# Kernel optimization log

Measured on AMD Instinct MI355X. Metric: run time of the kernel, lower is better.

Reference implementation:

```python
import jax, jax.numpy as jnp
import numpy as np
from jax import lax

THRESH = 0.8
LENS = 0.4
DECAY = 0.2
LOG_SIG_MIN, LOG_SIG_MAX = -20.0, 2.0
WINS = 15

@jax.custom_vjp
def act_fun(x):
    return (x > THRESH).astype(x.dtype)

def _act_fwd(x):
    return act_fun(x), x

def _act_bwd(x, g):
    return (g * (jnp.abs(x - THRESH) < LENS).astype(g.dtype),)

act_fun.defvjp(_act_fwd, _act_bwd)

B, NIN, HID, NACT = 2048, 512, 1024, 32

def _xavier(key, out_d, in_d):
    lim = jnp.sqrt(6.0 / (in_d + out_d)).astype(jnp.float32)
    return jax.random.uniform(key, (out_d, in_d), jnp.float32, -lim, lim)

def setup_inputs() -> dict:
    key = jax.random.key(0)
    ks = jax.random.split(key, 12)
    inp = {
        'state': jax.random.normal(ks[0], (B, 5, NIN), jnp.float32),
        'w1': _xavier(ks[1], HID, NIN), 'b1': jnp.zeros((HID,), jnp.float32),
        'w2': _xavier(ks[2], HID, NIN), 'b2': jnp.zeros((HID,), jnp.float32),
        'w3': _xavier(ks[3], HID, NIN), 'b3': jnp.zeros((HID,), jnp.float32),
        'wl': _xavier(ks[4], 1, 3), 'bl': jnp.zeros((1,), jnp.float32),
        'w11': _xavier(ks[5], HID, 4 * HID), 'b11': jnp.zeros((HID,), jnp.float32),
        'w12': _xavier(ks[6], HID, HID), 'b12': jnp.zeros((HID,), jnp.float32),
        'w21': _xavier(ks[7], HID, 4 * HID), 'b21': jnp.zeros((HID,), jnp.float32),
        'w22': _xavier(ks[8], HID, HID), 'b22': jnp.zeros((HID,), jnp.float32),
        'wm': _xavier(ks[9], NACT, HID), 'bm': jnp.zeros((NACT,), jnp.float32),
        'ws': _xavier(ks[10], NACT, HID), 'bs': jnp.zeros((NACT,), jnp.float32),
    }
    return inp

def _policy_forward(state, w1, b1, w2, b2, w3, b3, wl, bl,
                    w11, b11, w12, b12, w21, b21, w22, b22, wm, bm, ws, bs):
    batch = state.shape[0]
    hid = w1.shape[0]
    seq = jnp.repeat(state, 3, axis=1)
    mem0 = jnp.zeros((batch, hid, 4), state.dtype)
    sp0 = jnp.zeros((batch, hid, 4), state.dtype)

    def step(carry, x_t):
        mem, spike = carry
        i1 = x_t @ w1.T + b1  # [B, HID]
        i2 = x_t @ w2.T + b2
        i3 = x_t @ w3.T + b3
        inner = jnp.einsum('bck,k->bc', mem[:, :, :3], wl[0]) + bl[0]
        inp_all = jnp.stack([i1, i2, i3, inner], axis=-1)  # [B, HID, 4]
        mem1 = mem * DECAY * (1.0 - spike) + inp_all
        sp1 = act_fun(mem1)
        return (mem1, sp1), sp1

    _, spikes = lax.scan(step, (mem0, sp0), jnp.swapaxes(seq, 0, 1))  # [T,B,HID,4]
    spikes = jnp.transpose(spikes, (1, 0, 2, 3)).reshape(batch, WINS, hid * 4)
    x = jnp.mean(spikes, axis=1)  # [B, 4*HID]

    x1 = jax.nn.relu(x @ w11.T + b11)
    x1 = jax.nn.relu(x1 @ w12.T + b12)
    mean = x1 @ wm.T + bm

    x2 = jax.nn.relu(x @ w21.T + b21)
    x2 = jax.nn.relu(x2 @ w22.T + b22)
    log_std = jnp.clip(x2 @ ws.T + bs, LOG_SIG_MIN, LOG_SIG_MAX)
    return mean, log_std

def reference(state, w1, b1, w2, b2, w3, b3, wl, bl,
              w11, b11, w12, b12, w21, b21, w22, b22, wm, bm, ws, bs):
    return _policy_forward(state, w1, b1, w2, b2, w3, b3, wl, bl,
                           w11, b11, w12, b12, w21, b21, w22, b22, wm, bm, ws, bs)
```

## Files before the change

kernel.cpp:

```cpp
#include <hip/hip_runtime.h>
#include <cstddef>
#include <cstdint>

#define THRESH 0.8f
#define DECAY  0.2f

typedef unsigned short ushort_t;
typedef __attribute__((ext_vector_type(8))) short bf16x8;
typedef __attribute__((ext_vector_type(4))) float f32x4;

__device__ __forceinline__ ushort_t f2bf(float f) {
    union { float f; unsigned u; } v; v.f = f;
    unsigned r = v.u + 0x7FFFu + ((v.u >> 16) & 1u);
    return (ushort_t)(r >> 16);
}
__device__ __forceinline__ float bf2f(ushort_t h) {
    union { unsigned u; float f; } v; v.u = ((unsigned)h) << 16;
    return v.f;
}
__device__ __forceinline__ float blo(unsigned u) {
    union { unsigned x; float f; } v; v.x = u << 16; return v.f;
}
__device__ __forceinline__ float bhi(unsigned u) {
    union { unsigned x; float f; } v; v.x = u & 0xFFFF0000u; return v.f;
}

__device__ __forceinline__ void gload16(const void* g, void* l) {
    __builtin_amdgcn_global_load_lds(
        (const __attribute__((address_space(1))) void*)g,
        (__attribute__((address_space(3))) void*)l,
        16, 0, 0);
}

__global__ __launch_bounds__(512) void cur_gemm512(
    const ushort_t* __restrict__ Ah, const ushort_t* __restrict__ Al,
    const ushort_t* __restrict__ Wh, const ushort_t* __restrict__ Wl,
    const float* __restrict__ bias, float* __restrict__ C,
    int K, int ldc)
{
    __shared__ ushort_t sA[2][128 * 32];
    __shared__ ushort_t sW[2][128 * 32];

    const int t = threadIdx.x;
    const int mBase = blockIdx.x * 128;
    const int nBase = blockIdx.y * 128;

    const int lane = t & 63;
    const int wv = t >> 6;
    const int wm = (wv & 1) * 64;
    const int wn = (wv >> 1) * 32;
    const int fr = lane & 15;
    const int fq = lane >> 4;
    const int fsw = (fq ^ ((fr >> 2) & 3)) * 8;

    const int r0 = t >> 2;
    const int cSw = ((t & 3) ^ ((r0 >> 2) & 3)) * 8;

    f32x4 acc[4][2];
#pragma unroll
    for (int i = 0; i < 4; i++)
#pragma unroll
        for (int j = 0; j < 2; j++) {
            f32x4 z = {0.f, 0.f, 0.f, 0.f};
            acc[i][j] = z;
        }

    for (int k0 = 0; k0 < K; k0 += 32) {
        const int lin = t * 8;
        gload16(&Ah[(size_t)(mBase + r0) * K + k0 + cSw], &sA[0][lin]);
        gload16(&Wh[(size_t)(nBase + r0) * K + k0 + cSw], &sW[0][lin]);
        gload16(&Al[(size_t)(mBase + r0) * K + k0 + cSw], &sA[1][lin]);
        gload16(&Wl[(size_t)(nBase + r0) * K + k0 + cSw], &sW[1][lin]);
        __syncthreads();

        bf16x8 af[4][2], wf[2][2];
#pragma unroll
        for (int s = 0; s < 2; s++) {
#pragma unroll
            for (int i = 0; i < 4; i++)
                af[i][s] = *(const bf16x8*)&sA[s][(wm + i * 16 + fr) * 32 + fsw];
#pragma unroll
            for (int j = 0; j < 2; j++)
                wf[j][s] = *(const bf16x8*)&sW[s][(wn + j * 16 + fr) * 32 + fsw];
        }
#pragma unroll
        for (int i = 0; i < 4; i++)
#pragma unroll
            for (int j = 0; j < 2; j++) {
                acc[i][j] = __builtin_amdgcn_mfma_f32_16x16x32_bf16(af[i][0], wf[j][0], acc[i][j], 0, 0, 0);
                acc[i][j] = __builtin_amdgcn_mfma_f32_16x16x32_bf16(af[i][0], wf[j][1], acc[i][j], 0, 0, 0);
                acc[i][j] = __builtin_amdgcn_mfma_f32_16x16x32_bf16(af[i][1], wf[j][0], acc[i][j], 0, 0, 0);
            }
        __syncthreads();
    }

#pragma unroll
    for (int j = 0; j < 2; j++) {
        const int col = nBase + wn + j * 16 + fr;
        const float bv = bias[col];
#pragma unroll
        for (int i = 0; i < 4; i++)
#pragma unroll
            for (int r = 0; r < 4; r++) {
                const int row = mBase + wm + i * 16 + fq * 4 + r;
                C[(size_t)row * ldc + col] = acc[i][j][r] + bv;
            }
    }
}

__global__ __launch_bounds__(256) void mlp_gemm256(
    const ushort_t* __restrict__ A, const ushort_t* __restrict__ W,
    float* __restrict__ C,
    int N, int K, int lda, int ldw, int ldc, int aHalfOff,
    size_t sliceStride)
{
    __shared__ ushort_t sA[128 * 32];
    __shared__ ushort_t sW[128 * 32];

    const int t = threadIdx.x;
    const int mBase = blockIdx.x * 128;
    const int nBase = blockIdx.y * 128;
    const int kOff = blockIdx.z * K;
    const int aOff = (2 * nBase >= N) ? aHalfOff : 0;
    float* Cz = C + (size_t)blockIdx.z * sliceStride;

    const int lane = t & 63;
    const int wv = t >> 6;
    const int wm = (wv & 1) * 64;
    const int wn = (wv >> 1) * 64;
    const int fr = lane & 15;
    const int fq = lane >> 4;
    const int fsw = (fq ^ ((fr >> 2) & 3)) * 8;

    const int r0 = t >> 2;
    const int cSw = ((t & 3) ^ ((r0 >> 2) & 3)) * 8;

    f32x4 acc[4][4];
#pragma unroll
    for (int i = 0; i < 4; i++)
#pragma unroll
        for (int j = 0; j < 4; j++) {
            f32x4 z = {0.f, 0.f, 0.f, 0.f};
            acc[i][j] = z;
        }

    for (int k0 = 0; k0 < K; k0 += 32) {
        gload16(&A[(size_t)(mBase + r0) * lda + aOff + kOff + k0 + cSw], &sA[t * 8]);
        gload16(&A[(size_t)(mBase + 64 + r0) * lda + aOff + kOff + k0 + cSw], &sA[2048 + t * 8]);
        gload16(&W[(size_t)(nBase + r0) * ldw + kOff + k0 + cSw], &sW[t * 8]);
        gload16(&W[(size_t)(nBase + 64 + r0) * ldw + kOff + k0 + cSw], &sW[2048 + t * 8]);
        __syncthreads();

        bf16x8 af[4], wf[4];
#pragma unroll
        for (int i = 0; i < 4; i++) {
            af[i] = *(const bf16x8*)&sA[(wm + i * 16 + fr) * 32 + fsw];
            wf[i] = *(const bf16x8*)&sW[(wn + i * 16 + fr) * 32 + fsw];
        }
#pragma unroll
        for (int i = 0; i < 4; i++)
#pragma unroll
            for (int j = 0; j < 4; j++)
                acc[i][j] = __builtin_amdgcn_mfma_f32_16x16x32_bf16(af[i], wf[j], acc[i][j], 0, 0, 0);
        __syncthreads();
    }

#pragma unroll
    for (int j = 0; j < 4; j++) {
        const int col = nBase + wn + j * 16 + fr;
#pragma unroll
        for (int i = 0; i < 4; i++)
#pragma unroll
            for (int r = 0; r < 4; r++) {
                const int row = mBase + wm + i * 16 + fq * 4 + r;
                Cz[(size_t)row * ldc + col] = acc[i][j][r];
            }
    }
}

template <int S>
__global__ __launch_bounds__(256) void reduce_relu(
    const float* __restrict__ part, const float* __restrict__ bias,
    ushort_t* __restrict__ out, int N, size_t MN)
{
    const size_t stride = (size_t)gridDim.x * 1024;
    for (size_t e = ((size_t)blockIdx.x * 256 + threadIdx.x) * 4; e < MN; e += stride) {
        float4 a = *(const float4*)&part[e];
#pragma unroll
        for (int s = 1; s < S; s++) {
            const float4 b = *(const float4*)&part[s * MN + e];
            a.x += b.x; a.y += b.y; a.z += b.z; a.w += b.w;
        }
        const int n = (int)(e & (size_t)(N - 1));
        const float4 bv = *(const float4*)&bias[n];
        ushort4 o;
        o.x = f2bf(fmaxf(a.x + bv.x, 0.f));
        o.y = f2bf(fmaxf(a.y + bv.y, 0.f));
        o.z = f2bf(fmaxf(a.z + bv.z, 0.f));
        o.w = f2bf(fmaxf(a.w + bv.w, 0.f));
        *(ushort4*)&out[e] = o;
    }
}

__global__ __launch_bounds__(256) void recur_kernel(
    const float* __restrict__ cur, const float* __restrict__ wl,
    const float* __restrict__ bl, ushort_t* __restrict__ x)
{
    const int idx = blockIdx.x * 256 + threadIdx.x;
    const int b = idx >> 10, c = idx & 1023;
    const float wl0 = wl[0], wl1 = wl[1], wl2 = wl[2], bl0 = bl[0];
    float m0 = 0, m1 = 0, m2 = 0, m3 = 0;
    float s0 = 0, s1 = 0, s2 = 0, s3 = 0;
#pragma unroll
    for (int f = 0; f < 5; f++) {
        const float* p = cur + (size_t)(b * 5 + f) * 3072 + c;
        const float i1 = p[0], i2 = p[1024], i3 = p[2048];
#pragma unroll
        for (int rep = 0; rep < 3; rep++) {
            const float inner = m0 * wl0 + m1 * wl1 + m2 * wl2 + bl0;
            const float n0 = i1 + ((m0 > THRESH) ? 0.f : DECAY * m0);
            const float n1 = i2 + ((m1 > THRESH) ? 0.f : DECAY * m1);
            const float n2 = i3 + ((m2 > THRESH) ? 0.f : DECAY * m2);
            const float n3 = inner + ((m3 > THRESH) ? 0.f : DECAY * m3);
            m0 = n0; m1 = n1; m2 = n2; m3 = n3;
            s0 += (n0 > THRESH) ? 1.f : 0.f;
            s1 += (n1 > THRESH) ? 1.f : 0.f;
            s2 += (n2 > THRESH) ? 1.f : 0.f;
            s3 += (n3 > THRESH) ? 1.f : 0.f;
        }
    }
    const float inv = 1.f / 15.f;
    ushort4 o;
    o.x = f2bf(s0 * inv); o.y = f2bf(s1 * inv);
    o.z = f2bf(s2 * inv); o.w = f2bf(s3 * inv);
    *(ushort4*)&x[(size_t)b * 4096 + c * 4] = o;
}

__device__ __forceinline__ void do_split4(const float4* src, ushort4* hi,
                                          ushort4* lo, int base, int t) {
#pragma unroll
    for (int p = 0; p < 4; p++) {
        const int i = base * 1024 + p * 256 + t;
        const float4 v = src[i];
        ushort4 h, l;
        h.x = f2bf(v.x); l.x = f2bf(v.x - bf2f(h.x));
        h.y = f2bf(v.y); l.y = f2bf(v.y - bf2f(h.y));
        h.z = f2bf(v.z); l.z = f2bf(v.z - bf2f(h.z));
        h.w = f2bf(v.w); l.w = f2bf(v.w - bf2f(h.w));
        hi[i] = h; lo[i] = l;
    }
}
__device__ __forceinline__ void do_cvt4(const float4* src, ushort4* dst,
                                        int base, int t) {
#pragma unroll
    for (int p = 0; p < 4; p++) {
        const int i = base * 1024 + p * 256 + t;
        const float4 v = src[i];
        ushort4 h;
        h.x = f2bf(v.x); h.y = f2bf(v.y); h.z = f2bf(v.z); h.w = f2bf(v.w);
        dst[i] = h;
    }
}

__global__ __launch_bounds__(256) void prep_kernel(
    const float* __restrict__ state,
    const float* __restrict__ w1, const float* __restrict__ w2,
    const float* __restrict__ w3,
    const float* __restrict__ w11, const float* __restrict__ w21,
    const float* __restrict__ w12, const float* __restrict__ w22,
    const float* __restrict__ b1, const float* __restrict__ b2,
    const float* __restrict__ b3, const float* __restrict__ b11,
    const float* __restrict__ b21, const float* __restrict__ b12,
    const float* __restrict__ b22,
    ushort_t* __restrict__ sh, ushort_t* __restrict__ sl,
    ushort_t* __restrict__ wh123, ushort_t* __restrict__ wl123,
    ushort_t* __restrict__ w1b, ushort_t* __restrict__ w2b,
    float* __restrict__ b123, float* __restrict__ bb1, float* __restrict__ bb2)
{
    const int bid = blockIdx.x;
    const int t = threadIdx.x;
    if (bid < 1280) {
        do_split4((const float4*)state, (ushort4*)sh, (ushort4*)sl, bid, t);
    } else if (bid < 1408) {
        do_split4((const float4*)w1, (ushort4*)wh123, (ushort4*)wl123, bid - 1280, t);
    } else if (bid < 1536) {
        do_split4((const float4*)w2, (ushort4*)(wh123 + 524288),
                  (ushort4*)(wl123 + 524288), bid - 1408, t);
    } else if (bid < 1664) {
        do_split4((const float4*)w3, (ushort4*)(wh123 + 1048576),
                  (ushort4*)(wl123 + 1048576), bid - 1536, t);
    } else if (bid < 2688) {
        do_cvt4((const float4*)w11, (ushort4*)w1b, bid - 1664, t);
    } else if (bid < 3712) {
        do_cvt4((const float4*)w21, (ushort4*)(w1b + 4194304), bid - 2688, t);
    } else if (bid < 3968) {
        do_cvt4((const float4*)w12, (ushort4*)w2b, bid - 3712, t);
    } else if (bid < 4224) {
        do_cvt4((const float4*)w22, (ushort4*)(w2b + 1048576), bid - 3968, t);
    } else {
#pragma unroll
        for (int p = 0; p < 4; p++) {
            const int i = p * 256 + t;
            b123[i] = b1[i]; b123[1024 + i] = b2[i]; b123[2048 + i] = b3[i];
            bb1[i] = b11[i]; bb1[1024 + i] = b21[i];
            bb2[i] = b12[i]; bb2[1024 + i] = b22[i];
        }
    }
}

__global__ __launch_bounds__(256) void head_kernel(
    const ushort_t* __restrict__ h, const float* __restrict__ wm,
    const float* __restrict__ bm, const float* __restrict__ ws,
    const float* __restrict__ bs, float* __restrict__ out)
{
    const int t = threadIdx.x;
    const int branch = blockIdx.x >> 8;
    const int n = t & 31;
    const int b = (blockIdx.x & 255) * 8 + (t >> 5);
    const ushort_t* hr = h + (size_t)b * 2048 + branch * 1024;
    const float* wr = (branch ? ws : wm) + (size_t)n * 1024;
    float s = 0.f;
#pragma unroll 4
    for (int k = 0; k < 1024; k += 8) {
        const uint4 hv = *(const uint4*)&hr[k];
        const float4 w0 = *(const float4*)&wr[k];
        const float4 w1 = *(const float4*)&wr[k + 4];
        s += blo(hv.x) * w0.x + bhi(hv.x) * w0.y
           + blo(hv.y) * w0.z + bhi(hv.y) * w0.w
           + blo(hv.z) * w1.x + bhi(hv.z) * w1.y
           + blo(hv.w) * w1.z + bhi(hv.w) * w1.w;
    }
    s += (branch ? bs : bm)[n];
    if (branch) s = fminf(fmaxf(s, -20.f), 2.f);
    out[(size_t)branch * 65536 + (size_t)b * 32 + n] = s;
}

extern "C" void kernel_launch(void* const* d_in, const int* in_sizes, int n_in,
                              void* d_out, int out_size, void* d_ws, size_t ws_size,
                              hipStream_t stream)
{
    const float* state = (const float*)d_in[0];
    const float* w1  = (const float*)d_in[1];  const float* b1  = (const float*)d_in[2];
    const float* w2  = (const float*)d_in[3];  const float* b2  = (const float*)d_in[4];
    const float* w3  = (const float*)d_in[5];  const float* b3  = (const float*)d_in[6];
    const float* wl  = (const float*)d_in[7];  const float* bl  = (const float*)d_in[8];
    const float* w11 = (const float*)d_in[9];  const float* b11 = (const float*)d_in[10];
    const float* w12 = (const float*)d_in[11]; const float* b12 = (const float*)d_in[12];
    const float* w21 = (const float*)d_in[13]; const float* b21 = (const float*)d_in[14];
    const float* w22 = (const float*)d_in[15]; const float* b22 = (const float*)d_in[16];
    const float* wm  = (const float*)d_in[17]; const float* bm  = (const float*)d_in[18];
    const float* ws  = (const float*)d_in[19]; const float* bs  = (const float*)d_in[20];
    float* out = (float*)d_out;

    char* wp = (char*)d_ws;
    float*    cur   = (float*)wp;     wp += (size_t)10240 * 3072 * 4;
    ushort_t* sh    = (ushort_t*)wp;  wp += (size_t)10240 * 512 * 2;
    ushort_t* sl    = (ushort_t*)wp;  wp += (size_t)10240 * 512 * 2;
    ushort_t* wh123 = (ushort_t*)wp;  wp += (size_t)3072 * 512 * 2;
    ushort_t* wl123 = (ushort_t*)wp;  wp += (size_t)3072 * 512 * 2;
    ushort_t* xb    = (ushort_t*)wp;  wp += (size_t)2048 * 4096 * 2;
    ushort_t* w1b   = (ushort_t*)wp;  wp += (size_t)2048 * 4096 * 2;
    ushort_t* w2b   = (ushort_t*)wp;  wp += (size_t)2048 * 1024 * 2;
    ushort_t* h1    = (ushort_t*)wp;  wp += (size_t)2048 * 2048 * 2;
    ushort_t* h2    = (ushort_t*)wp;  wp += (size_t)2048 * 2048 * 2;
    float*    b123  = (float*)wp;     wp += 3072 * 4;
    float*    bb1   = (float*)wp;     wp += 2048 * 4;
    float*    bb2   = (float*)wp;     wp += 2048 * 4;

    const size_t MN = (size_t)2048 * 2048;

    prep_kernel<<<4225, 256, 0, stream>>>(
        state, w1, w2, w3, w11, w21, w12, w22,
        b1, b2, b3, b11, b21, b12, b22,
        sh, sl, wh123, wl123, w1b, w2b, b123, bb1, bb2);

    cur_gemm512<<<dim3(80, 24), 512, 0, stream>>>(
        sh, sl, wh123, wl123, b123, cur, 512, 3072);

    recur_kernel<<<8192, 256, 0, stream>>>(cur, wl, bl, xb);

    mlp_gemm256<<<dim3(16, 16, 2), 256, 0, stream>>>(
        xb, w1b, cur, 2048, 2048, 4096, 4096, 2048, 0, MN);
    reduce_relu<2><<<1024, 256, 0, stream>>>(cur, bb1, h1, 2048, MN);

    mlp_gemm256<<<dim3(16, 16, 2), 256, 0, stream>>>(
        h1, w2b, cur, 2048, 512, 2048, 1024, 2048, 1024, MN);
    reduce_relu<2><<<1024, 256, 0, stream>>>(cur, bb2, h2, 2048, MN);

    head_kernel<<<512, 256, 0, stream>>>(h2, wm, bm, ws, bs, out);
}
```

Before: 435.6 us.

## Fuse input-current GEMM with spiking recurrence and drop LDS swizzle in MLP GEMM

The split-bf16 GEMM that produces the three input currents is merged with the LIF recurrence. Each block computes a 320-row by 96-column tile (64 batch rows × 5 frames, 32 channels × 3 weights) and runs the recurrence from shared memory, so the large fp32 `cur` tensor is never written to or read back from global memory. This removes a kernel launch and the intermediate traffic. In exchange the new tile shape gives lower MFMA reuse per block, the epilogue serialises four staging passes through LDS with barriers, and the LDS layout has no XOR swizzle, so bank conflicts are possible. Separately, the XOR swizzle in the MLP GEMM's LDS layout is replaced with a plain linear layout, which may add bank conflicts.

```diff
diff --git a/kernel.cpp b/kernel.cpp
--- a/kernel.cpp
+++ b/kernel.cpp
@@ -32,79 +32,128 @@
         16, 0, 0);
 }
 
-__global__ __launch_bounds__(512) void cur_gemm512(
+__global__ __launch_bounds__(512) void cur_recur_fused(
     const ushort_t* __restrict__ Ah, const ushort_t* __restrict__ Al,
     const ushort_t* __restrict__ Wh, const ushort_t* __restrict__ Wl,
-    const float* __restrict__ bias, float* __restrict__ C,
-    int K, int ldc)
-{
-    __shared__ ushort_t sA[2][128 * 32];
-    __shared__ ushort_t sW[2][128 * 32];
+    const float* __restrict__ b123, const float* __restrict__ wl,
+    const float* __restrict__ bl, ushort_t* __restrict__ x)
+{
+    __shared__ ushort_t smem[26624];
+    ushort_t* sAh = smem;
+    ushort_t* sAl = smem + 10240;
+    ushort_t* sWh = smem + 20480;
+    ushort_t* sWl = smem + 23552;
 
     const int t = threadIdx.x;
-    const int mBase = blockIdx.x * 128;
-    const int nBase = blockIdx.y * 128;
-
     const int lane = t & 63;
     const int wv = t >> 6;
-    const int wm = (wv & 1) * 64;
-    const int wn = (wv >> 1) * 32;
+    const int cBase = blockIdx.x * 32;
+    const int bBase = blockIdx.y * 64;
+    const int aRow0 = bBase * 5;
+
+    const int mg = wv & 3;
+    const int ng = wv >> 2;
     const int fr = lane & 15;
     const int fq = lane >> 4;
-    const int fsw = (fq ^ ((fr >> 2) & 3)) * 8;
-
-    const int r0 = t >> 2;
-    const int cSw = ((t & 3) ^ ((r0 >> 2) & 3)) * 8;
-
-    f32x4 acc[4][2];
-#pragma unroll
-    for (int i = 0; i < 4; i++)
-#pragma unroll
-        for (int j = 0; j < 2; j++) {
+    const int rlane = lane >> 2;
+    const int klane = (lane & 3) * 8;
+
+    f32x4 acc[5][3];
+#pragma unroll
+    for (int i = 0; i < 5; i++)
+#pragma unroll
+        for (int j = 0; j < 3; j++) {
             f32x4 z = {0.f, 0.f, 0.f, 0.f};
             acc[i][j] = z;
         }
 
-    for (int k0 = 0; k0 < K; k0 += 32) {
-        const int lin = t * 8;
-        gload16(&Ah[(size_t)(mBase + r0) * K + k0 + cSw], &sA[0][lin]);
-        gload16(&Wh[(size_t)(nBase + r0) * K + k0 + cSw], &sW[0][lin]);
-        gload16(&Al[(size_t)(mBase + r0) * K + k0 + cSw], &sA[1][lin]);
-        gload16(&Wl[(size_t)(nBase + r0) * K + k0 + cSw], &sW[1][lin]);
-        __syncthreads();
-
-        bf16x8 af[4][2], wf[2][2];
-#pragma unroll
-        for (int s = 0; s < 2; s++) {
-#pragma unroll
-            for (int i = 0; i < 4; i++)
-                af[i][s] = *(const bf16x8*)&sA[s][(wm + i * 16 + fr) * 32 + fsw];
-#pragma unroll
-            for (int j = 0; j < 2; j++)
-                wf[j][s] = *(const bf16x8*)&sW[s][(wn + j * 16 + fr) * 32 + fsw];
-        }
-#pragma unroll
-        for (int i = 0; i < 4; i++)
-#pragma unroll
-            for (int j = 0; j < 2; j++) {
-                acc[i][j] = __builtin_amdgcn_mfma_f32_16x16x32_bf16(af[i][0], wf[j][0], acc[i][j], 0, 0, 0);
-                acc[i][j] = __builtin_amdgcn_mfma_f32_16x16x32_bf16(af[i][0], wf[j][1], acc[i][j], 0, 0, 0);
-                acc[i][j] = __builtin_amdgcn_mfma_f32_16x16x32_bf16(af[i][1], wf[j][0], acc[i][j], 0, 0, 0);
+    for (int k0 = 0; k0 < 512; k0 += 32) {
+        for (int s = wv; s < 52; s += 8) {
+            if (s < 40) {
+                const int ss = (s < 20) ? s : s - 20;
+                const ushort_t* src = (s < 20) ? Ah : Al;
+                ushort_t* dst = (s < 20) ? sAh : sAl;
+                const int row = aRow0 + ss * 16 + rlane;
+                gload16(&src[(size_t)row * 512 + k0 + klane], &dst[ss * 512 + lane * 8]);
+            } else {
+                const int ss = (s < 46) ? s - 40 : s - 46;
+                const ushort_t* src = (s < 46) ? Wh : Wl;
+                ushort_t* dst = (s < 46) ? sWh : sWl;
+                const int wrow = ss * 16 + rlane;
+                const int row = (wrow >> 5) * 1024 + cBase + (wrow & 31);
+                gload16(&src[(size_t)row * 512 + k0 + klane], &dst[ss * 512 + lane * 8]);
             }
-        __syncthreads();
-    }
-
-#pragma unroll
-    for (int j = 0; j < 2; j++) {
-        const int col = nBase + wn + j * 16 + fr;
-        const float bv = bias[col];
-#pragma unroll
-        for (int i = 0; i < 4; i++)
-#pragma unroll
-            for (int r = 0; r < 4; r++) {
-                const int row = mBase + wm + i * 16 + fq * 4 + r;
-                C[(size_t)row * ldc + col] = acc[i][j][r] + bv;
+        }
+        __syncthreads();
+
+        bf16x8 wf[3][2];
+#pragma unroll
+        for (int j = 0; j < 3; j++) {
+            wf[j][0] = *(const bf16x8*)&sWh[(ng * 48 + j * 16 + fr) * 32 + fq * 8];
+            wf[j][1] = *(const bf16x8*)&sWl[(ng * 48 + j * 16 + fr) * 32 + fq * 8];
+        }
+#pragma unroll
+        for (int i = 0; i < 5; i++) {
+            const bf16x8 ah = *(const bf16x8*)&sAh[(mg * 80 + i * 16 + fr) * 32 + fq * 8];
+            const bf16x8 al = *(const bf16x8*)&sAl[(mg * 80 + i * 16 + fr) * 32 + fq * 8];
+#pragma unroll
+            for (int j = 0; j < 3; j++) {
+                acc[i][j] = __builtin_amdgcn_mfma_f32_16x16x32_bf16(ah, wf[j][0], acc[i][j], 0, 0, 0);
+                acc[i][j] = __builtin_amdgcn_mfma_f32_16x16x32_bf16(ah, wf[j][1], acc[i][j], 0, 0, 0);
+                acc[i][j] = __builtin_amdgcn_mfma_f32_16x16x32_bf16(al, wf[j][0], acc[i][j], 0, 0, 0);
             }
+        }
+        __syncthreads();
+    }
+
+    float* buf = (float*)smem;
+    const float wl0 = wl[0], wl1 = wl[1], wl2 = wl[2], bl0 = bl[0];
+    const int lb = t >> 5;
+    const int lc = t & 31;
+    const float bv0 = b123[cBase + lc];
+    const float bv1 = b123[1024 + cBase + lc];
+    const float bv2 = b123[2048 + cBase + lc];
+    const float inv15 = 1.0f / 15.0f;
+
+    for (int q = 0; q < 4; q++) {
+        if (mg == q) {
+#pragma unroll
+            for (int i = 0; i < 5; i++)
+#pragma unroll
+                for (int j = 0; j < 3; j++)
+#pragma unroll
+                    for (int r = 0; r < 4; r++)
+                        buf[(i * 16 + fq * 4 + r) * 96 + ng * 48 + j * 16 + fr] = acc[i][j][r];
+        }
+        __syncthreads();
+
+        float m0 = 0, m1 = 0, m2 = 0, m3 = 0;
+        float s0 = 0, s1 = 0, s2 = 0, s3 = 0;
+#pragma unroll
+        for (int f = 0; f < 5; f++) {
+            const float* p = &buf[(lb * 5 + f) * 96 + lc];
+            const float i1 = p[0] + bv0;
+            const float i2 = p[32] + bv1;
+            const float i3 = p[64] + bv2;
+#pragma unroll
+            for (int rep = 0; rep < 3; rep++) {
+                const float inner = m0 * wl0 + m1 * wl1 + m2 * wl2 + bl0;
+                const float n0 = i1 + ((m0 > THRESH) ? 0.f : DECAY * m0);
+                const float n1 = i2 + ((m1 > THRESH) ? 0.f : DECAY * m1);
+                const float n2 = i3 + ((m2 > THRESH) ? 0.f : DECAY * m2);
+                const float n3 = inner + ((m3 > THRESH) ? 0.f : DECAY * m3);
+                m0 = n0; m1 = n1; m2 = n2; m3 = n3;
+                s0 += (n0 > THRESH) ? 1.f : 0.f;
+                s1 += (n1 > THRESH) ? 1.f : 0.f;
+                s2 += (n2 > THRESH) ? 1.f : 0.f;
+                s3 += (n3 > THRESH) ? 1.f : 0.f;
+            }
+        }
+        ushort4 o;
+        o.x = f2bf(s0 * inv15); o.y = f2bf(s1 * inv15);
+        o.z = f2bf(s2 * inv15); o.w = f2bf(s3 * inv15);
+        *(ushort4*)&x[(size_t)(bBase + q * 16 + lb) * 4096 + (cBase + lc) * 4] = o;
+        __syncthreads();
     }
 }
 
@@ -130,10 +179,9 @@
     const int wn = (wv >> 1) * 64;
     const int fr = lane & 15;
     const int fq = lane >> 4;
-    const int fsw = (fq ^ ((fr >> 2) & 3)) * 8;
 
     const int r0 = t >> 2;
-    const int cSw = ((t & 3) ^ ((r0 >> 2) & 3)) * 8;
+    const int cc = (t & 3) * 8;
 
     f32x4 acc[4][4];
 #pragma unroll
@@ -145,17 +193,17 @@
         }
 
     for (int k0 = 0; k0 < K; k0 += 32) {
-        gload16(&A[(size_t)(mBase + r0) * lda + aOff + kOff + k0 + cSw], &sA[t * 8]);
-        gload16(&A[(size_t)(mBase + 64 + r0) * lda + aOff + kOff + k0 + cSw], &sA[2048 + t * 8]);
-        gload16(&W[(size_t)(nBase + r0) * ldw + kOff + k0 + cSw], &sW[t * 8]);
-        gload16(&W[(size_t)(nBase + 64 + r0) * ldw + kOff + k0 + cSw], &sW[2048 + t * 8]);
+        gload16(&A[(size_t)(mBase + r0) * lda + aOff + kOff + k0 + cc], &sA[t * 8]);
+        gload16(&A[(size_t)(mBase + 64 + r0) * lda + aOff + kOff + k0 + cc], &sA[2048 + t * 8]);
+        gload16(&W[(size_t)(nBase + r0) * ldw + kOff + k0 + cc], &sW[t * 8]);
+        gload16(&W[(size_t)(nBase + 64 + r0) * ldw + kOff + k0 + cc], &sW[2048 + t * 8]);
         __syncthreads();
 
         bf16x8 af[4], wf[4];
 #pragma unroll
         for (int i = 0; i < 4; i++) {
-            af[i] = *(const bf16x8*)&sA[(wm + i * 16 + fr) * 32 + fsw];
-            wf[i] = *(const bf16x8*)&sW[(wn + i * 16 + fr) * 32 + fsw];
+            af[i] = *(const bf16x8*)&sA[(wm + i * 16 + fr) * 32 + fq * 8];
+            wf[i] = *(const bf16x8*)&sW[(wn + i * 16 + fr) * 32 + fq * 8];
         }
 #pragma unroll
         for (int i = 0; i < 4; i++)
@@ -200,40 +248,6 @@
         o.w = f2bf(fmaxf(a.w + bv.w, 0.f));
         *(ushort4*)&out[e] = o;
     }
-}
-
-__global__ __launch_bounds__(256) void recur_kernel(
-    const float* __restrict__ cur, const float* __restrict__ wl,
-    const float* __restrict__ bl, ushort_t* __restrict__ x)
-{
-    const int idx = blockIdx.x * 256 + threadIdx.x;
-    const int b = idx >> 10, c = idx & 1023;
-    const float wl0 = wl[0], wl1 = wl[1], wl2 = wl[2], bl0 = bl[0];
-    float m0 = 0, m1 = 0, m2 = 0, m3 = 0;
-    float s0 = 0, s1 = 0, s2 = 0, s3 = 0;
-#pragma unroll
-    for (int f = 0; f < 5; f++) {
-        const float* p = cur + (size_t)(b * 5 + f) * 3072 + c;
-        const float i1 = p[0], i2 = p[1024], i3 = p[2048];
-#pragma unroll
-        for (int rep = 0; rep < 3; rep++) {
-            const float inner = m0 * wl0 + m1 * wl1 + m2 * wl2 + bl0;
-            const float n0 = i1 + ((m0 > THRESH) ? 0.f : DECAY * m0);
-            const float n1 = i2 + ((m1 > THRESH) ? 0.f : DECAY * m1);
-            const float n2 = i3 + ((m2 > THRESH) ? 0.f : DECAY * m2);
-            const float n3 = inner + ((m3 > THRESH) ? 0.f : DECAY * m3);
-            m0 = n0; m1 = n1; m2 = n2; m3 = n3;
-            s0 += (n0 > THRESH) ? 1.f : 0.f;
-            s1 += (n1 > THRESH) ? 1.f : 0.f;
-            s2 += (n2 > THRESH) ? 1.f : 0.f;
-            s3 += (n3 > THRESH) ? 1.f : 0.f;
-        }
-    }
-    const float inv = 1.f / 15.f;
-    ushort4 o;
-    o.x = f2bf(s0 * inv); o.y = f2bf(s1 * inv);
-    o.z = f2bf(s2 * inv); o.w = f2bf(s3 * inv);
-    *(ushort4*)&x[(size_t)b * 4096 + c * 4] = o;
 }
 
 __device__ __forceinline__ void do_split4(const float4* src, ushort4* hi,
@@ -374,10 +388,8 @@
         b1, b2, b3, b11, b21, b12, b22,
         sh, sl, wh123, wl123, w1b, w2b, b123, bb1, bb2);
 
-    cur_gemm512<<<dim3(80, 24), 512, 0, stream>>>(
-        sh, sl, wh123, wl123, b123, cur, 512, 3072);
-
-    recur_kernel<<<8192, 256, 0, stream>>>(cur, wl, bl, xb);
+    cur_recur_fused<<<dim3(32, 32), 512, 0, stream>>>(
+        sh, sl, wh123, wl123, b123, wl, bl, xb);
 
     mlp_gemm256<<<dim3(16, 16, 2), 256, 0, stream>>>(
         xb, w1b, cur, 2048, 2048, 4096, 4096, 2048, 0, MN);
```

Result: slower. 451.3 us (+3.6%).

## Drop split-K with fused bias-ReLU epilogue and retile current GEMM

Applied to the files above, without the earlier changes.

The two MLP GEMMs no longer use split-K with a separate reduce_relu pass. They now use 64x128 tiles with a full-K loop and apply bias, ReLU and the bf16 conversion directly in the epilogue, which removes the fp32 partial writes and two extra kernel launches. The input-current GEMM moves from 512 threads with 64x32 warp tiles to 256 threads with 64x64 warp tiles, which raises MFMA work per LDS read. The XOR LDS swizzle is removed in both kernels, so shared-memory bank conflicts may increase. Longer K loops per block also reduce the available parallelism.

```diff
diff --git a/kernel.cpp b/kernel.cpp
--- a/kernel.cpp
+++ b/kernel.cpp
@@ -32,97 +32,19 @@
         16, 0, 0);
 }
 
-__global__ __launch_bounds__(512) void cur_gemm512(
+__global__ __launch_bounds__(256) void cur_gemm256(
     const ushort_t* __restrict__ Ah, const ushort_t* __restrict__ Al,
     const ushort_t* __restrict__ Wh, const ushort_t* __restrict__ Wl,
-    const float* __restrict__ bias, float* __restrict__ C,
-    int K, int ldc)
-{
-    __shared__ ushort_t sA[2][128 * 32];
-    __shared__ ushort_t sW[2][128 * 32];
+    const float* __restrict__ bias, float* __restrict__ C, int ldc)
+{
+    __shared__ ushort_t sAh[128 * 32];
+    __shared__ ushort_t sAl[128 * 32];
+    __shared__ ushort_t sWh[128 * 32];
+    __shared__ ushort_t sWl[128 * 32];
 
     const int t = threadIdx.x;
     const int mBase = blockIdx.x * 128;
     const int nBase = blockIdx.y * 128;
-
-    const int lane = t & 63;
-    const int wv = t >> 6;
-    const int wm = (wv & 1) * 64;
-    const int wn = (wv >> 1) * 32;
-    const int fr = lane & 15;
-    const int fq = lane >> 4;
-    const int fsw = (fq ^ ((fr >> 2) & 3)) * 8;
-
-    const int r0 = t >> 2;
-    const int cSw = ((t & 3) ^ ((r0 >> 2) & 3)) * 8;
-
-    f32x4 acc[4][2];
-#pragma unroll
-    for (int i = 0; i < 4; i++)
-#pragma unroll
-        for (int j = 0; j < 2; j++) {
-            f32x4 z = {0.f, 0.f, 0.f, 0.f};
-            acc[i][j] = z;
-        }
-
-    for (int k0 = 0; k0 < K; k0 += 32) {
-        const int lin = t * 8;
-        gload16(&Ah[(size_t)(mBase + r0) * K + k0 + cSw], &sA[0][lin]);
-        gload16(&Wh[(size_t)(nBase + r0) * K + k0 + cSw], &sW[0][lin]);
-        gload16(&Al[(size_t)(mBase + r0) * K + k0 + cSw], &sA[1][lin]);
-        gload16(&Wl[(size_t)(nBase + r0) * K + k0 + cSw], &sW[1][lin]);
-        __syncthreads();
-
-        bf16x8 af[4][2], wf[2][2];
-#pragma unroll
-        for (int s = 0; s < 2; s++) {
-#pragma unroll
-            for (int i = 0; i < 4; i++)
-                af[i][s] = *(const bf16x8*)&sA[s][(wm + i * 16 + fr) * 32 + fsw];
-#pragma unroll
-            for (int j = 0; j < 2; j++)
-                wf[j][s] = *(const bf16x8*)&sW[s][(wn + j * 16 + fr) * 32 + fsw];
-        }
-#pragma unroll
-        for (int i = 0; i < 4; i++)
-#pragma unroll
-            for (int j = 0; j < 2; j++) {
-                acc[i][j] = __builtin_amdgcn_mfma_f32_16x16x32_bf16(af[i][0], wf[j][0], acc[i][j], 0, 0, 0);
-                acc[i][j] = __builtin_amdgcn_mfma_f32_16x16x32_bf16(af[i][0], wf[j][1], acc[i][j], 0, 0, 0);
-                acc[i][j] = __builtin_amdgcn_mfma_f32_16x16x32_bf16(af[i][1], wf[j][0], acc[i][j], 0, 0, 0);
-            }
-        __syncthreads();
-    }
-
-#pragma unroll
-    for (int j = 0; j < 2; j++) {
-        const int col = nBase + wn + j * 16 + fr;
-        const float bv = bias[col];
-#pragma unroll
-        for (int i = 0; i < 4; i++)
-#pragma unroll
-            for (int r = 0; r < 4; r++) {
-                const int row = mBase + wm + i * 16 + fq * 4 + r;
-                C[(size_t)row * ldc + col] = acc[i][j][r] + bv;
-            }
-    }
-}
-
-__global__ __launch_bounds__(256) void mlp_gemm256(
-    const ushort_t* __restrict__ A, const ushort_t* __restrict__ W,
-    float* __restrict__ C,
-    int N, int K, int lda, int ldw, int ldc, int aHalfOff,
-    size_t sliceStride)
-{
-    __shared__ ushort_t sA[128 * 32];
-    __shared__ ushort_t sW[128 * 32];
-
-    const int t = threadIdx.x;
-    const int mBase = blockIdx.x * 128;
-    const int nBase = blockIdx.y * 128;
-    const int kOff = blockIdx.z * K;
-    const int aOff = (2 * nBase >= N) ? aHalfOff : 0;
-    float* Cz = C + (size_t)blockIdx.z * sliceStride;
 
     const int lane = t & 63;
     const int wv = t >> 6;
@@ -130,10 +52,9 @@
     const int wn = (wv >> 1) * 64;
     const int fr = lane & 15;
     const int fq = lane >> 4;
-    const int fsw = (fq ^ ((fr >> 2) & 3)) * 8;
 
     const int r0 = t >> 2;
-    const int cSw = ((t & 3) ^ ((r0 >> 2) & 3)) * 8;
+    const int cc = (t & 3) * 8;
 
     f32x4 acc[4][4];
 #pragma unroll
@@ -144,61 +65,113 @@
             acc[i][j] = z;
         }
 
+    for (int k0 = 0; k0 < 512; k0 += 32) {
+        gload16(&Ah[(size_t)(mBase + r0) * 512 + k0 + cc], &sAh[t * 8]);
+        gload16(&Ah[(size_t)(mBase + 64 + r0) * 512 + k0 + cc], &sAh[2048 + t * 8]);
+        gload16(&Al[(size_t)(mBase + r0) * 512 + k0 + cc], &sAl[t * 8]);
+        gload16(&Al[(size_t)(mBase + 64 + r0) * 512 + k0 + cc], &sAl[2048 + t * 8]);
+        gload16(&Wh[(size_t)(nBase + r0) * 512 + k0 + cc], &sWh[t * 8]);
+        gload16(&Wh[(size_t)(nBase + 64 + r0) * 512 + k0 + cc], &sWh[2048 + t * 8]);
+        gload16(&Wl[(size_t)(nBase + r0) * 512 + k0 + cc], &sWl[t * 8]);
+        gload16(&Wl[(size_t)(nBase + 64 + r0) * 512 + k0 + cc], &sWl[2048 + t * 8]);
+        __syncthreads();
+
+        bf16x8 af[4][2], wf[4][2];
+#pragma unroll
+        for (int i = 0; i < 4; i++) {
+            af[i][0] = *(const bf16x8*)&sAh[(wm + i * 16 + fr) * 32 + fq * 8];
+            af[i][1] = *(const bf16x8*)&sAl[(wm + i * 16 + fr) * 32 + fq * 8];
+            wf[i][0] = *(const bf16x8*)&sWh[(wn + i * 16 + fr) * 32 + fq * 8];
+            wf[i][1] = *(const bf16x8*)&sWl[(wn + i * 16 + fr) * 32 + fq * 8];
+        }
+#pragma unroll
+        for (int i = 0; i < 4; i++)
+#pragma unroll
+            for (int j = 0; j < 4; j++) {
+                acc[i][j] = __builtin_amdgcn_mfma_f32_16x16x32_bf16(af[i][0], wf[j][0], acc[i][j], 0, 0, 0);
+                acc[i][j] = __builtin_amdgcn_mfma_f32_16x16x32_bf16(af[i][0], wf[j][1], acc[i][j], 0, 0, 0);
+                acc[i][j] = __builtin_amdgcn_mfma_f32_16x16x32_bf16(af[i][1], wf[j][0], acc[i][j], 0, 0, 0);
+            }
+        __syncthreads();
+    }
+
+#pragma unroll
+    for (int j = 0; j < 4; j++) {
+        const int col = nBase + wn + j * 16 + fr;
+        const float bv = bias[col];
+#pragma unroll
+        for (int i = 0; i < 4; i++)
+#pragma unroll
+            for (int r = 0; r < 4; r++) {
+                const int row = mBase + wm + i * 16 + fq * 4 + r;
+                C[(size_t)row * ldc + col] = acc[i][j][r] + bv;
+            }
+    }
+}
+
+__global__ __launch_bounds__(256) void mlp_gemm(
+    const ushort_t* __restrict__ A, const ushort_t* __restrict__ W,
+    const float* __restrict__ bias, ushort_t* __restrict__ C,
+    int N, int K, int lda, int ldw, int ldc, int aHalfOff)
+{
+    __shared__ ushort_t sA[64 * 32];
+    __shared__ ushort_t sW[128 * 32];
+
+    const int t = threadIdx.x;
+    const int mBase = blockIdx.x * 64;
+    const int nBase = blockIdx.y * 128;
+    const int aOff = (2 * nBase >= N) ? aHalfOff : 0;
+
+    const int lane = t & 63;
+    const int wv = t >> 6;
+    const int wn = wv * 32;
+    const int fr = lane & 15;
+    const int fq = lane >> 4;
+
+    const int r0 = t >> 2;
+    const int cc = (t & 3) * 8;
+
+    f32x4 acc[4][2];
+#pragma unroll
+    for (int i = 0; i < 4; i++)
+#pragma unroll
+        for (int j = 0; j < 2; j++) {
+            f32x4 z = {0.f, 0.f, 0.f, 0.f};
+            acc[i][j] = z;
+        }
+
     for (int k0 = 0; k0 < K; k0 += 32) {
-        gload16(&A[(size_t)(mBase + r0) * lda + aOff + kOff + k0 + cSw], &sA[t * 8]);
-        gload16(&A[(size_t)(mBase + 64 + r0) * lda + aOff + kOff + k0 + cSw], &sA[2048 + t * 8]);
-        gload16(&W[(size_t)(nBase + r0) * ldw + kOff + k0 + cSw], &sW[t * 8]);
-        gload16(&W[(size_t)(nBase + 64 + r0) * ldw + kOff + k0 + cSw], &sW[2048 + t * 8]);
+        gload16(&A[(size_t)(mBase + r0) * lda + aOff + k0 + cc], &sA[t * 8]);
+        gload16(&W[(size_t)(nBase + r0) * ldw + k0 + cc], &sW[t * 8]);
+        gload16(&W[(size_t)(nBase + 64 + r0) * ldw + k0 + cc], &sW[2048 + t * 8]);
         __syncthreads();
 
-        bf16x8 af[4], wf[4];
-#pragma unroll
-        for (int i = 0; i < 4; i++) {
-            af[i] = *(const bf16x8*)&sA[(wm + i * 16 + fr) * 32 + fsw];
-            wf[i] = *(const bf16x8*)&sW[(wn + i * 16 + fr) * 32 + fsw];
-        }
-#pragma unroll
-        for (int i = 0; i < 4; i++)
-#pragma unroll
-            for (int j = 0; j < 4; j++)
+        bf16x8 af[4], wf[2];
+#pragma unroll
+        for (int i = 0; i < 4; i++)
+            af[i] = *(const bf16x8*)&sA[(i * 16 + fr) * 32 + fq * 8];
+#pragma unroll
+        for (int j = 0; j < 2; j++)
+            wf[j] = *(const bf16x8*)&sW[(wn + j * 16 + fr) * 32 + fq * 8];
+#pragma unroll
+        for (int i = 0; i < 4; i++)
+#pragma unroll
+            for (int j = 0; j < 2; j++)
                 acc[i][j] = __builtin_amdgcn_mfma_f32_16x16x32_bf16(af[i], wf[j], acc[i][j], 0, 0, 0);
         __syncthreads();
     }
 
 #pragma unroll
-    for (int j = 0; j < 4; j++) {
+    for (int j = 0; j < 2; j++) {
         const int col = nBase + wn + j * 16 + fr;
+        const float bv = bias[col];
 #pragma unroll
         for (int i = 0; i < 4; i++)
 #pragma unroll
             for (int r = 0; r < 4; r++) {
-                const int row = mBase + wm + i * 16 + fq * 4 + r;
-                Cz[(size_t)row * ldc + col] = acc[i][j][r];
+                const int row = mBase + i * 16 + fq * 4 + r;
+                C[(size_t)row * ldc + col] = f2bf(fmaxf(acc[i][j][r] + bv, 0.f));
             }
-    }
-}
-
-template <int S>
-__global__ __launch_bounds__(256) void reduce_relu(
-    const float* __restrict__ part, const float* __restrict__ bias,
-    ushort_t* __restrict__ out, int N, size_t MN)
-{
-    const size_t stride = (size_t)gridDim.x * 1024;
-    for (size_t e = ((size_t)blockIdx.x * 256 + threadIdx.x) * 4; e < MN; e += stride) {
-        float4 a = *(const float4*)&part[e];
-#pragma unroll
-        for (int s = 1; s < S; s++) {
-            const float4 b = *(const float4*)&part[s * MN + e];
-            a.x += b.x; a.y += b.y; a.z += b.z; a.w += b.w;
-        }
-        const int n = (int)(e & (size_t)(N - 1));
-        const float4 bv = *(const float4*)&bias[n];
-        ushort4 o;
-        o.x = f2bf(fmaxf(a.x + bv.x, 0.f));
-        o.y = f2bf(fmaxf(a.y + bv.y, 0.f));
-        o.z = f2bf(fmaxf(a.z + bv.z, 0.f));
-        o.w = f2bf(fmaxf(a.w + bv.w, 0.f));
-        *(ushort4*)&out[e] = o;
     }
 }
 
@@ -367,25 +340,21 @@
     float*    bb1   = (float*)wp;     wp += 2048 * 4;
     float*    bb2   = (float*)wp;     wp += 2048 * 4;
 
-    const size_t MN = (size_t)2048 * 2048;
-
     prep_kernel<<<4225, 256, 0, stream>>>(
         state, w1, w2, w3, w11, w21, w12, w22,
         b1, b2, b3, b11, b21, b12, b22,
         sh, sl, wh123, wl123, w1b, w2b, b123, bb1, bb2);
 
-    cur_gemm512<<<dim3(80, 24), 512, 0, stream>>>(
-        sh, sl, wh123, wl123, b123, cur, 512, 3072);
+    cur_gemm256<<<dim3(80, 24), 256, 0, stream>>>(
+        sh, sl, wh123, wl123, b123, cur, 3072);
 
     recur_kernel<<<8192, 256, 0, stream>>>(cur, wl, bl, xb);
 
-    mlp_gemm256<<<dim3(16, 16, 2), 256, 0, stream>>>(
-        xb, w1b, cur, 2048, 2048, 4096, 4096, 2048, 0, MN);
-    reduce_relu<2><<<1024, 256, 0, stream>>>(cur, bb1, h1, 2048, MN);
-
-    mlp_gemm256<<<dim3(16, 16, 2), 256, 0, stream>>>(
-        h1, w2b, cur, 2048, 512, 2048, 1024, 2048, 1024, MN);
-    reduce_relu<2><<<1024, 256, 0, stream>>>(cur, bb2, h2, 2048, MN);
+    mlp_gemm<<<dim3(32, 16), 256, 0, stream>>>(
+        xb, w1b, bb1, h1, 2048, 4096, 4096, 4096, 2048, 0);
+
+    mlp_gemm<<<dim3(32, 16), 256, 0, stream>>>(
+        h1, w2b, bb2, h2, 2048, 1024, 2048, 1024, 2048, 1024);
 
     head_kernel<<<512, 256, 0, stream>>>(h2, wm, bm, ws, bs, out);
 }
```

Measured after the change: 421.9 us. 3.1% less time.

## Raise split-K for first MLP GEMM, drop LDS swizzle, flatten reduce kernel

Applied to the files above, without the earlier changes.

The first MLP GEMM now splits K four ways instead of two, doubling the block count to fill more CUs. reduce_relu becomes one float4 per thread with a larger grid, with a 4-way sum for that layer. The XOR swizzle on LDS stores and loads in both GEMM kernels is removed in favour of plain row-major offsets, which simplifies address math. The costs are more partial-sum traffic to global memory and likely LDS bank conflicts on the fragment reads.

```diff
diff --git a/kernel.cpp b/kernel.cpp
--- a/kernel.cpp
+++ b/kernel.cpp
@@ -51,10 +51,9 @@
     const int wn = (wv >> 1) * 32;
     const int fr = lane & 15;
     const int fq = lane >> 4;
-    const int fsw = (fq ^ ((fr >> 2) & 3)) * 8;
 
     const int r0 = t >> 2;
-    const int cSw = ((t & 3) ^ ((r0 >> 2) & 3)) * 8;
+    const int cc = (t & 3) * 8;
 
     f32x4 acc[4][2];
 #pragma unroll
@@ -67,10 +66,10 @@
 
     for (int k0 = 0; k0 < K; k0 += 32) {
         const int lin = t * 8;
-        gload16(&Ah[(size_t)(mBase + r0) * K + k0 + cSw], &sA[0][lin]);
-        gload16(&Wh[(size_t)(nBase + r0) * K + k0 + cSw], &sW[0][lin]);
-        gload16(&Al[(size_t)(mBase + r0) * K + k0 + cSw], &sA[1][lin]);
-        gload16(&Wl[(size_t)(nBase + r0) * K + k0 + cSw], &sW[1][lin]);
+        gload16(&Ah[(size_t)(mBase + r0) * K + k0 + cc], &sA[0][lin]);
+        gload16(&Wh[(size_t)(nBase + r0) * K + k0 + cc], &sW[0][lin]);
+        gload16(&Al[(size_t)(mBase + r0) * K + k0 + cc], &sA[1][lin]);
+        gload16(&Wl[(size_t)(nBase + r0) * K + k0 + cc], &sW[1][lin]);
         __syncthreads();
 
         bf16x8 af[4][2], wf[2][2];
@@ -78,10 +77,10 @@
         for (int s = 0; s < 2; s++) {
 #pragma unroll
             for (int i = 0; i < 4; i++)
-                af[i][s] = *(const bf16x8*)&sA[s][(wm + i * 16 + fr) * 32 + fsw];
+                af[i][s] = *(const bf16x8*)&sA[s][(wm + i * 16 + fr) * 32 + fq * 8];
 #pragma unroll
             for (int j = 0; j < 2; j++)
-                wf[j][s] = *(const bf16x8*)&sW[s][(wn + j * 16 + fr) * 32 + fsw];
+                wf[j][s] = *(const bf16x8*)&sW[s][(wn + j * 16 + fr) * 32 + fq * 8];
         }
 #pragma unroll
         for (int i = 0; i < 4; i++)
@@ -130,10 +129,9 @@
     const int wn = (wv >> 1) * 64;
     const int fr = lane & 15;
     const int fq = lane >> 4;
-    const int fsw = (fq ^ ((fr >> 2) & 3)) * 8;
 
     const int r0 = t >> 2;
-    const int cSw = ((t & 3) ^ ((r0 >> 2) & 3)) * 8;
+    const int cc = (t & 3) * 8;
 
     f32x4 acc[4][4];
 #pragma unroll
@@ -145,17 +143,17 @@
         }
 
     for (int k0 = 0; k0 < K; k0 += 32) {
-        gload16(&A[(size_t)(mBase + r0) * lda + aOff + kOff + k0 + cSw], &sA[t * 8]);
-        gload16(&A[(size_t)(mBase + 64 + r0) * lda + aOff + kOff + k0 + cSw], &sA[2048 + t * 8]);
-        gload16(&W[(size_t)(nBase + r0) * ldw + kOff + k0 + cSw], &sW[t * 8]);
-        gload16(&W[(size_t)(nBase + 64 + r0) * ldw + kOff + k0 + cSw], &sW[2048 + t * 8]);
+        gload16(&A[(size_t)(mBase + r0) * lda + aOff + kOff + k0 + cc], &sA[t * 8]);
+        gload16(&A[(size_t)(mBase + 64 + r0) * lda + aOff + kOff + k0 + cc], &sA[2048 + t * 8]);
+        gload16(&W[(size_t)(nBase + r0) * ldw + kOff + k0 + cc], &sW[t * 8]);
+        gload16(&W[(size_t)(nBase + 64 + r0) * ldw + kOff + k0 + cc], &sW[2048 + t * 8]);
         __syncthreads();
 
         bf16x8 af[4], wf[4];
 #pragma unroll
         for (int i = 0; i < 4; i++) {
-            af[i] = *(const bf16x8*)&sA[(wm + i * 16 + fr) * 32 + fsw];
-            wf[i] = *(const bf16x8*)&sW[(wn + i * 16 + fr) * 32 + fsw];
+            af[i] = *(const bf16x8*)&sA[(wm + i * 16 + fr) * 32 + fq * 8];
+            wf[i] = *(const bf16x8*)&sW[(wn + i * 16 + fr) * 32 + fq * 8];
         }
 #pragma unroll
         for (int i = 0; i < 4; i++)
@@ -183,23 +181,22 @@
     const float* __restrict__ part, const float* __restrict__ bias,
     ushort_t* __restrict__ out, int N, size_t MN)
 {
-    const size_t stride = (size_t)gridDim.x * 1024;
-    for (size_t e = ((size_t)blockIdx.x * 256 + threadIdx.x) * 4; e < MN; e += stride) {
-        float4 a = *(const float4*)&part[e];
-#pragma unroll
-        for (int s = 1; s < S; s++) {
-            const float4 b = *(const float4*)&part[s * MN + e];
-            a.x += b.x; a.y += b.y; a.z += b.z; a.w += b.w;
-        }
-        const int n = (int)(e & (size_t)(N - 1));
-        const float4 bv = *(const float4*)&bias[n];
-        ushort4 o;
-        o.x = f2bf(fmaxf(a.x + bv.x, 0.f));
-        o.y = f2bf(fmaxf(a.y + bv.y, 0.f));
-        o.z = f2bf(fmaxf(a.z + bv.z, 0.f));
-        o.w = f2bf(fmaxf(a.w + bv.w, 0.f));
-        *(ushort4*)&out[e] = o;
-    }
+    const size_t e = ((size_t)blockIdx.x * 256 + threadIdx.x) * 4;
+    if (e >= MN) return;
+    float4 a = *(const float4*)&part[e];
+#pragma unroll
+    for (int s = 1; s < S; s++) {
+        const float4 b = *(const float4*)&part[s * MN + e];
+        a.x += b.x; a.y += b.y; a.z += b.z; a.w += b.w;
+    }
+    const int n = (int)(e & (size_t)(N - 1));
+    const float4 bv = *(const float4*)&bias[n];
+    ushort4 o;
+    o.x = f2bf(fmaxf(a.x + bv.x, 0.f));
+    o.y = f2bf(fmaxf(a.y + bv.y, 0.f));
+    o.z = f2bf(fmaxf(a.z + bv.z, 0.f));
+    o.w = f2bf(fmaxf(a.w + bv.w, 0.f));
+    *(ushort4*)&out[e] = o;
 }
 
 __global__ __launch_bounds__(256) void recur_kernel(
@@ -379,13 +376,13 @@
 
     recur_kernel<<<8192, 256, 0, stream>>>(cur, wl, bl, xb);
 
-    mlp_gemm256<<<dim3(16, 16, 2), 256, 0, stream>>>(
-        xb, w1b, cur, 2048, 2048, 4096, 4096, 2048, 0, MN);
-    reduce_relu<2><<<1024, 256, 0, stream>>>(cur, bb1, h1, 2048, MN);
+    mlp_gemm256<<<dim3(16, 16, 4), 256, 0, stream>>>(
+        xb, w1b, cur, 2048, 1024, 4096, 4096, 2048, 0, MN);
+    reduce_relu<4><<<4096, 256, 0, stream>>>(cur, bb1, h1, 2048, MN);
 
     mlp_gemm256<<<dim3(16, 16, 2), 256, 0, stream>>>(
         h1, w2b, cur, 2048, 512, 2048, 1024, 2048, 1024, MN);
-    reduce_relu<2><<<1024, 256, 0, stream>>>(cur, bb2, h2, 2048, MN);
+    reduce_relu<2><<<4096, 256, 0, stream>>>(cur, bb2, h2, 2048, MN);
 
     head_kernel<<<512, 256, 0, stream>>>(h2, wm, bm, ws, bs, out);
 }
```

New measurement: 413.8 us. 5.0% less time.
